# Kernel tuning notes

Hardware: AMD Instinct MI355X
Metric: run time of the kernel (lower is better)

## Reference

```python
import jax, jax.numpy as jnp
import numpy as np
from jax import lax

B, N, D, S, K = 8, 4096, 61, 1024, 32
MLP = (64, 64, 128)
WN = (3, 8, 8, 16)  # WeightNet: 3 -> 8 -> 8 -> 16
EPS = 1e-5


def _gather(p, idx):
    # p: [B, N, C], idx: [B, ...] -> [B, ..., C]
    return jax.vmap(lambda pb, ib: pb[ib])(p, idx)


def _fps(xyz, npoint, key):
    # farthest point sampling, xyz: [B, N, 3] -> idx [B, npoint]
    b, n, _ = xyz.shape
    start = jax.random.randint(key, (b,), 0, n)
    def step(carry, _):
        dmin, far = carry
        centroid = jnp.take_along_axis(xyz, far[:, None, None], axis=1)  # [B,1,3]
        d = jnp.sum((xyz - centroid) ** 2, -1)                            # [B,N]
        dmin = jnp.minimum(dmin, d)
        return (dmin, jnp.argmax(dmin, -1)), far
    _, idxs = lax.scan(step, (jnp.full((b, n), 1e10, xyz.dtype), start), None, length=npoint)
    return idxs.T  # [B, npoint]


def _sqdist(a, b):
    # a: [B,S,3], b: [B,N,3] -> [B,S,N]
    return (jnp.sum(a ** 2, -1)[:, :, None] + jnp.sum(b ** 2, -1)[:, None, :]
            - 2.0 * jnp.einsum('bsc,bnc->bsn', a, b))


def _bn_relu(x, g, be):
    # channels-last BN (training-mode batch stats, biased var) + ReLU
    axes = tuple(range(x.ndim - 1))
    m = x.mean(axes, keepdims=True)
    v = x.var(axes, keepdims=True)
    return jax.nn.relu(g * (x - m) * lax.rsqrt(v + EPS) + be)


def _forward(xyz, points, mlp_p, wn_p, lin_w, lin_b, bnl_g, bnl_b):
    xyz_t = xyz.transpose(0, 2, 1)    # [B,N,3]
    pts = points.transpose(0, 2, 1)   # [B,N,D]
    xyz_sg = lax.stop_gradient(xyz_t)  # index computations carry no grads (as in torch)
    fps_idx = _fps(xyz_sg, S, jax.random.key(42))  # [B,S]
    new_xyz = _gather(xyz_t, fps_idx)              # [B,S,3]
    idx = lax.top_k(-_sqdist(lax.stop_gradient(new_xyz), xyz_sg), K)[1]  # [B,S,K]
    g_norm = _gather(xyz_t, idx) - new_xyz[:, :, None, :]                # [B,S,K,3]
    feat = jnp.concatenate([g_norm, _gather(pts, idx)], -1)              # [B,S,K,3+D]
    for w, b, g, be in mlp_p:
        feat = _bn_relu(jnp.einsum('bskc,oc->bsko', feat, w) + b, g, be)
    wts = g_norm
    for w, b, g, be in wn_p:
        wts = _bn_relu(jnp.einsum('bskc,oc->bsko', wts, w) + b, g, be)   # [B,S,K,16]
    # [B,S,C,K] @ [B,S,K,16] -> [B,S,C,16] -> [B,S,C*16] (C-major flatten, as torch .view)
    agg = jnp.einsum('bskc,bskw->bscw', feat, wts).reshape(B, S, -1)
    out = agg @ lin_w.T + lin_b                                          # [B,S,128]
    m = out.mean((0, 1), keepdims=True)  # BatchNorm1d over batch and spatial
    v = out.var((0, 1), keepdims=True)
    out = jax.nn.relu(bnl_g * (out - m) * lax.rsqrt(v + EPS) + bnl_b)
    return new_xyz.transpose(0, 2, 1), out.transpose(0, 2, 1)  # [B,3,S], [B,128,S]


def setup_inputs() -> dict:
    key = jax.random.key(0)
    ks = iter(jax.random.split(key, 64))
    inp = {"xyz": jax.random.normal(next(ks), (B, 3, N), jnp.float32),
           "points": jax.random.normal(next(ks), (B, D, N), jnp.float32)}
    mlp_in = (3 + D,) + MLP[:-1]
    for i, (ci, co) in enumerate(zip(mlp_in, MLP)):
        inp[f"mlp_w{i}"] = jax.random.normal(next(ks), (co, ci), jnp.float32) / np.float32(np.sqrt(ci))
        inp[f"mlp_b{i}"] = jnp.zeros((co,), jnp.float32)
        inp[f"mlp_g{i}"] = jnp.ones((co,), jnp.float32)
        inp[f"mlp_be{i}"] = jnp.zeros((co,), jnp.float32)
    for i, (ci, co) in enumerate(zip(WN[:-1], WN[1:])):
        inp[f"wn_w{i}"] = jax.random.normal(next(ks), (co, ci), jnp.float32) / np.float32(np.sqrt(ci))
        inp[f"wn_b{i}"] = jnp.zeros((co,), jnp.float32)
        inp[f"wn_g{i}"] = jnp.ones((co,), jnp.float32)
        inp[f"wn_be{i}"] = jnp.zeros((co,), jnp.float32)
    fin = 16 * MLP[-1]
    inp["lin_w"] = jax.random.normal(next(ks), (MLP[-1], fin), jnp.float32) / np.float32(np.sqrt(fin))
    inp["lin_b"] = jnp.zeros((MLP[-1],), jnp.float32)
    inp["bnl_g"] = jnp.ones((MLP[-1],), jnp.float32)
    inp["bnl_b"] = jnp.zeros((MLP[-1],), jnp.float32)
    return inp


def reference(xyz, points, mlp_w0, mlp_b0, mlp_g0, mlp_be0, mlp_w1, mlp_b1, mlp_g1, mlp_be1, mlp_w2, mlp_b2, mlp_g2, mlp_be2, wn_w0, wn_b0, wn_g0, wn_be0, wn_w1, wn_b1, wn_g1, wn_be1, wn_w2, wn_b2, wn_g2, wn_be2, lin_w, lin_b, bnl_g, bnl_b):
    mlp_p = [(mlp_w0, mlp_b0, mlp_g0, mlp_be0),
             (mlp_w1, mlp_b1, mlp_g1, mlp_be1),
             (mlp_w2, mlp_b2, mlp_g2, mlp_be2)]
    wn_p = [(wn_w0, wn_b0, wn_g0, wn_be0),
            (wn_w1, wn_b1, wn_g1, wn_be1),
            (wn_w2, wn_b2, wn_g2, wn_be2)]
    return _forward(xyz, points, mlp_p, wn_p, lin_w, lin_b, bnl_g, bnl_b)
```

## Files before the change

kernel.cpp:

```cpp
#include <hip/hip_runtime.h>
#include <cstdint>
#include <cstddef>


constexpr int B_ = 8, N_ = 4096, D_ = 61, S_ = 1024, K_ = 32;
constexpr int P_ = B_ * S_ * K_;
constexpr int BS_ = B_ * S_;

constexpr size_t OFF_STATS  = 0;
constexpr size_t OFF_FPSIDX = 8192;
constexpr size_t OFF_NEWXYZ = 40960;
constexpr size_t OFF_KNN    = 139264;
constexpr size_t OFF_PT     = 1187840;
constexpr size_t OFF_Y01    = 9183232;
constexpr size_t OFF_Y2     = 76292096;
constexpr size_t OFF_W01    = 210509824;
constexpr size_t OFF_W2B    = 218898432;
constexpr size_t OFF_OUTPRE = 235675648;

static inline uint32_t rotl32(uint32_t x, int r){ return (x << r) | (x >> (32 - r)); }
static void tf2x32(uint32_t k0, uint32_t k1, uint32_t x0, uint32_t x1,
                   uint32_t* o0, uint32_t* o1){
  uint32_t ks[3] = {k0, k1, k0 ^ k1 ^ 0x1BD11BDAu};
  x0 += ks[0]; x1 += ks[1];
  const int RA[4] = {13,15,26,6}, RB[4] = {17,29,16,24};
  for (int i = 0; i < 5; ++i){
    const int* R = (i & 1) ? RB : RA;
    for (int j = 0; j < 4; ++j){ x0 += x1; x1 = rotl32(x1, R[j]); x1 ^= x0; }
    x0 += ks[(i+1)%3]; x1 += ks[(i+2)%3] + (uint32_t)(i+1);
  }
  *o0 = x0; *o1 = x1;
}
struct StartIdx { int v[8]; };
static StartIdx compute_starts(){
  uint32_t ka, kb;
  tf2x32(0u, 42u, 0u, 1u, &ka, &kb);
  StartIdx s;
  for (int i = 0; i < 8; ++i){
    uint32_t b1, b2;
    tf2x32(ka, kb, 0u, (uint32_t)i, &b1, &b2);
    s.v[i] = (int)((b1 ^ b2) & 4095u);
  }
  return s;
}

__global__ __launch_bounds__(64) void tr_kernel(const float* __restrict__ pts,
                                                float* __restrict__ pT){
  __shared__ float tile[61][65];
  const int b = blockIdx.x >> 6;
  const int n0 = (blockIdx.x & 63) * 64;
  const int t = threadIdx.x;
  for (int d = 0; d < 61; ++d)
    tile[d][t] = pts[((size_t)b*61 + d)*N_ + n0 + t];
  __syncthreads();
  float* dst = pT + ((size_t)b*N_ + n0 + t)*61;
  for (int d = 0; d < 61; ++d) dst[d] = tile[d][t];
}

#define REP8(M) M(0) M(1) M(2) M(3) M(4) M(5) M(6) M(7)

__global__ __launch_bounds__(512, 1) void fps_kernel(const float* __restrict__ xyz,
                                                     StartIdx st,
                                                     float* __restrict__ new_xyz,
                                                     float* __restrict__ out_xyz){
  const int b = blockIdx.x, tid = threadIdx.x;
  const int lane = tid & 63, wv = tid >> 6;
  const float* xb = xyz + (size_t)b*3*N_;
  __shared__ float4 pts4[N_];
  __shared__ unsigned long long slots[2][8];

#define LOADP(i) \
  float px##i = xb[tid + 512*(i)]; \
  float py##i = xb[N_ + tid + 512*(i)]; \
  float pz##i = xb[2*N_ + tid + 512*(i)]; \
  float dm##i = 1e10f; \
  pts4[tid + 512*(i)] = make_float4(px##i, py##i, pz##i, 0.f);
  REP8(LOADP)
#undef LOADP
  __syncthreads();

  const int start = st.v[b];
  float4 c4 = pts4[start];
  float cx = c4.x, cy = c4.y, cz = c4.z;

  int par = 0;
  for (int s = 0; s < S_; ++s){
    if (tid == 0){
      new_xyz[((size_t)b*S_ + s)*3 + 0] = cx;
      new_xyz[((size_t)b*S_ + s)*3 + 1] = cy;
      new_xyz[((size_t)b*S_ + s)*3 + 2] = cz;
      out_xyz[(size_t)b*3*S_ + s]        = cx;
      out_xyz[(size_t)b*3*S_ + S_ + s]   = cy;
      out_xyz[(size_t)b*3*S_ + 2*S_ + s] = cz;
    }
#define UPD(i) \
    unsigned long long key##i; { \
      float dx = __fsub_rn(px##i, cx), dy = __fsub_rn(py##i, cy), dz = __fsub_rn(pz##i, cz); \
      float d  = __fadd_rn(__fadd_rn(__fmul_rn(dx,dx), __fmul_rn(dy,dy)), __fmul_rn(dz,dz)); \
      dm##i = fminf(dm##i, d); \
      key##i = ((unsigned long long)__float_as_uint(dm##i) << 32) \
             | (unsigned int)(~(unsigned int)(tid + 512*(i))); }
    REP8(UPD)
#undef UPD
    unsigned long long t0 = key0 > key1 ? key0 : key1;
    unsigned long long t1 = key2 > key3 ? key2 : key3;
    unsigned long long t2 = key4 > key5 ? key4 : key5;
    unsigned long long t3 = key6 > key7 ? key6 : key7;
    unsigned long long u0 = t0 > t1 ? t0 : t1;
    unsigned long long u1 = t2 > t3 ? t2 : t3;
    unsigned long long k  = u0 > u1 ? u0 : u1;
#pragma unroll
    for (int off = 32; off >= 1; off >>= 1){
      unsigned long long o = __shfl_xor(k, off);
      if (o > k) k = o;
    }
    if (lane == 0) slots[par][wv] = k;
    __syncthreads();
    unsigned long long bk = slots[par][0];
    { unsigned long long v1 = slots[par][1]; if (v1 > bk) bk = v1;
      unsigned long long v2 = slots[par][2]; if (v2 > bk) bk = v2;
      unsigned long long v3 = slots[par][3]; if (v3 > bk) bk = v3;
      unsigned long long v4 = slots[par][4]; if (v4 > bk) bk = v4;
      unsigned long long v5 = slots[par][5]; if (v5 > bk) bk = v5;
      unsigned long long v6 = slots[par][6]; if (v6 > bk) bk = v6;
      unsigned long long v7 = slots[par][7]; if (v7 > bk) bk = v7; }
    const int winner = (int)(~(unsigned int)bk) & (N_ - 1);
    float4 w4 = pts4[winner];
    cx = w4.x; cy = w4.y; cz = w4.z;
    par ^= 1;
  }
}
#undef REP8

__global__ __launch_bounds__(256) void knn_kernel(const float* __restrict__ xyz,
                                                  const float* __restrict__ nxyz,
                                                  int* __restrict__ knn_idx){
  __shared__ float dist[4][4096];
  const int wv = threadIdx.x >> 6, lane = threadIdx.x & 63;
  const int q = blockIdx.x*4 + wv;
  const int b = q >> 10;
  const float* xb = xyz + (size_t)b*3*N_;
  const float ax = nxyz[(size_t)q*3], ay = nxyz[(size_t)q*3+1], az = nxyz[(size_t)q*3+2];
  const float sa = __fadd_rn(__fadd_rn(__fmul_rn(ax,ax), __fmul_rn(ay,ay)), __fmul_rn(az,az));
  float* dw = dist[wv];
  float lv = 3.4e38f; int ln = 0;
  for (int i = 0; i < 64; ++i){
    int n = i*64 + lane;
    float x = xb[n], y = xb[N_+n], z = xb[2*N_+n];
    float sb  = __fadd_rn(__fadd_rn(__fmul_rn(x,x), __fmul_rn(y,y)), __fmul_rn(z,z));
    float dot = __fadd_rn(__fadd_rn(__fmul_rn(ax,x), __fmul_rn(ay,y)), __fmul_rn(az,z));
    float d   = __fsub_rn(__fadd_rn(sa, sb), __fmul_rn(2.f, dot));
    dw[n] = d;
    if (d < lv){ lv = d; ln = n; }
  }
  __syncthreads();
  int myout = 0;
  for (int r = 0; r < 32; ++r){
    float gv = lv; int gn = ln;
#pragma unroll
    for (int off = 32; off >= 1; off >>= 1){
      float ov = __shfl_xor(gv, off); int on = __shfl_xor(gn, off);
      if (ov < gv || (ov == gv && on < gn)){ gv = ov; gn = on; }
    }
    if (lane == r) myout = gn;
    const int col = gn & 63, row = gn >> 6;
    float v = dw[lane*64 + col];
    if (lane == row){ v = 3.4e38f; dw[lane*64 + col] = 3.4e38f; }
    float nv = v; int nn = lane*64 + col;
#pragma unroll
    for (int off = 32; off >= 1; off >>= 1){
      float ov = __shfl_xor(nv, off); int on = __shfl_xor(nn, off);
      if (ov < nv || (ov == nv && on < nn)){ nv = ov; nn = on; }
    }
    if (lane == col){ lv = nv; ln = nn; }
  }
  if (lane < 32) knn_idx[(size_t)q*32 + lane] = myout;
}

__global__ __launch_bounds__(256, 2) void m0_kernel(const float* __restrict__ pT,
                                                    const float* __restrict__ xyz,
                                                    const float* __restrict__ nxyz,
                                                    const int* __restrict__ knn_idx,
                                                    const float* __restrict__ w,
                                                    const float* __restrict__ bias,
                                                    float* __restrict__ y){
  __shared__ float Wt[4096]; __shared__ float bb[64];
  for (int t = threadIdx.x; t < 4096; t += 256){ int o = t >> 6, c = t & 63; Wt[c*64+o] = w[o*64+c]; }
  if (threadIdx.x < 64) bb[threadIdx.x] = bias[threadIdx.x];
  __syncthreads();
  const int p = blockIdx.x*256 + threadIdx.x;
  const int b = p >> 15, s = (p & 32767) >> 5;
  const int n = knn_idx[p];
  float in[64];
  {
    const float* xb = xyz + (size_t)b*3*N_;
    const int q = (b << 10) + s;
    in[0] = xb[n]       - nxyz[(size_t)q*3];
    in[1] = xb[N_+n]    - nxyz[(size_t)q*3+1];
    in[2] = xb[2*N_+n]  - nxyz[(size_t)q*3+2];
    const float* pr = pT + ((size_t)b*N_ + n)*61;
#pragma unroll
    for (int d = 0; d < 61; ++d) in[3+d] = pr[d];
  }
  float acc[64];
#pragma unroll
  for (int o = 0; o < 64; ++o) acc[o] = bb[o];
#pragma unroll
  for (int c = 0; c < 64; ++c){
    float x = in[c];
#pragma unroll
    for (int o = 0; o < 64; o += 4){
      float4 w4 = *reinterpret_cast<const float4*>(&Wt[c*64+o]);
      acc[o]   += x*w4.x; acc[o+1] += x*w4.y; acc[o+2] += x*w4.z; acc[o+3] += x*w4.w;
    }
  }
#pragma unroll
  for (int o = 0; o < 64; ++o) y[(size_t)o*P_ + p] = acc[o];
}

__global__ __launch_bounds__(256) void stats_kernel(const float* __restrict__ y,
                                                    double* __restrict__ st, int C){
  const int c = blockIdx.x % C, chunk = blockIdx.x / C;
  const float* row = y + (size_t)c*P_ + (size_t)chunk*32768;
  double s = 0.0, q = 0.0;
  for (int i = threadIdx.x; i < 32768; i += 256){ double v = row[i]; s += v; q += v*v; }
  __shared__ double ss[256], qq[256];
  ss[threadIdx.x] = s; qq[threadIdx.x] = q; __syncthreads();
  for (int w = 128; w >= 1; w >>= 1){
    if (threadIdx.x < w){ ss[threadIdx.x] += ss[threadIdx.x+w]; qq[threadIdx.x] += qq[threadIdx.x+w]; }
    __syncthreads();
  }
  if (threadIdx.x == 0){ atomicAdd(&st[c*2], ss[0]); atomicAdd(&st[c*2+1], qq[0]); }
}

__device__ __forceinline__ void bn_coeff(const double* st, const float* g, const float* be,
                                         int c, double cnt, float* sc, float* sh){
  double mean = st[c*2] / cnt;
  double var  = st[c*2+1] / cnt - mean*mean;
  double scale = (double)g[c] / sqrt(var + 1e-5);
  *sc = (float)scale; *sh = (float)((double)be[c] - mean*scale);
}

__global__ __launch_bounds__(256, 2) void m1_kernel(float* __restrict__ y,
                                                    const float* __restrict__ w,
                                                    const float* __restrict__ bias,
                                                    const double* __restrict__ st,
                                                    const float* __restrict__ g,
                                                    const float* __restrict__ be){
  __shared__ float Wt[4096]; __shared__ float bb[64], sc[64], sh[64];
  for (int t = threadIdx.x; t < 4096; t += 256){ int o = t >> 6, c = t & 63; Wt[c*64+o] = w[o*64+c]; }
  if (threadIdx.x < 64){
    bn_coeff(st, g, be, threadIdx.x, (double)P_, &sc[threadIdx.x], &sh[threadIdx.x]);
    bb[threadIdx.x] = bias[threadIdx.x];
  }
  __syncthreads();
  const int p = blockIdx.x*256 + threadIdx.x;
  float in[64];
#pragma unroll
  for (int c = 0; c < 64; ++c){
    float x = y[(size_t)c*P_ + p];
    in[c] = fmaxf(0.f, fmaf(x, sc[c], sh[c]));
  }
  float acc[64];
#pragma unroll
  for (int o = 0; o < 64; ++o) acc[o] = bb[o];
#pragma unroll
  for (int c = 0; c < 64; ++c){
    float x = in[c];
#pragma unroll
    for (int o = 0; o < 64; o += 4){
      float4 w4 = *reinterpret_cast<const float4*>(&Wt[c*64+o]);
      acc[o]   += x*w4.x; acc[o+1] += x*w4.y; acc[o+2] += x*w4.z; acc[o+3] += x*w4.w;
    }
  }
#pragma unroll
  for (int o = 0; o < 64; ++o) y[(size_t)o*P_ + p] = acc[o];
}

__global__ __launch_bounds__(256, 2) void m2_kernel(const float* __restrict__ y1,
                                                    float* __restrict__ y2,
                                                    const float* __restrict__ w,
                                                    const float* __restrict__ bias,
                                                    const double* __restrict__ st,
                                                    const float* __restrict__ g,
                                                    const float* __restrict__ be){
  __shared__ float Wt[4096]; __shared__ float bb[64], sc[64], sh[64];
  const int half = blockIdx.y;
  for (int t = threadIdx.x; t < 4096; t += 256){
    int o = t >> 6, c = t & 63;
    Wt[c*64+o] = w[(size_t)(half*64+o)*64 + c];
  }
  if (threadIdx.x < 64){
    bn_coeff(st, g, be, threadIdx.x, (double)P_, &sc[threadIdx.x], &sh[threadIdx.x]);
    bb[threadIdx.x] = bias[half*64 + threadIdx.x];
  }
  __syncthreads();
  const int p = blockIdx.x*256 + threadIdx.x;
  float in[64];
#pragma unroll
  for (int c = 0; c < 64; ++c){
    float x = y1[(size_t)c*P_ + p];
    in[c] = fmaxf(0.f, fmaf(x, sc[c], sh[c]));
  }
  float acc[64];
#pragma unroll
  for (int o = 0; o < 64; ++o) acc[o] = bb[o];
#pragma unroll
  for (int c = 0; c < 64; ++c){
    float x = in[c];
#pragma unroll
    for (int o = 0; o < 64; o += 4){
      float4 w4 = *reinterpret_cast<const float4*>(&Wt[c*64+o]);
      acc[o]   += x*w4.x; acc[o+1] += x*w4.y; acc[o+2] += x*w4.z; acc[o+3] += x*w4.w;
    }
  }
#pragma unroll
  for (int o = 0; o < 64; ++o) y2[(size_t)(half*64+o)*P_ + p] = acc[o];
}

__global__ __launch_bounds__(256) void w0_kernel(const float* __restrict__ xyz,
                                                 const float* __restrict__ nxyz,
                                                 const int* __restrict__ knn_idx,
                                                 const float* __restrict__ w,
                                                 const float* __restrict__ bias,
                                                 float* __restrict__ wb){
  __shared__ float Wl[24], bb[8];
  if (threadIdx.x < 24) Wl[threadIdx.x] = w[threadIdx.x];
  if (threadIdx.x < 8)  bb[threadIdx.x] = bias[threadIdx.x];
  __syncthreads();
  const int p = blockIdx.x*256 + threadIdx.x;
  const int b = p >> 15, s = (p & 32767) >> 5;
  const int n = knn_idx[p];
  const float* xb = xyz + (size_t)b*3*N_;
  const int q = (b << 10) + s;
  float gx = xb[n]      - nxyz[(size_t)q*3];
  float gy = xb[N_+n]   - nxyz[(size_t)q*3+1];
  float gz = xb[2*N_+n] - nxyz[(size_t)q*3+2];
#pragma unroll
  for (int o = 0; o < 8; ++o){
    float a = bb[o] + gx*Wl[o*3] + gy*Wl[o*3+1] + gz*Wl[o*3+2];
    wb[(size_t)o*P_ + p] = a;
  }
}

__global__ __launch_bounds__(256) void w1_kernel(float* __restrict__ wb,
                                                 const float* __restrict__ w,
                                                 const float* __restrict__ bias,
                                                 const double* __restrict__ st,
                                                 const float* __restrict__ g,
                                                 const float* __restrict__ be){
  __shared__ float Wl[64], bb[8], sc[8], sh[8];
  if (threadIdx.x < 64) Wl[threadIdx.x] = w[threadIdx.x];
  if (threadIdx.x < 8){
    bn_coeff(st, g, be, threadIdx.x, (double)P_, &sc[threadIdx.x], &sh[threadIdx.x]);
    bb[threadIdx.x] = bias[threadIdx.x];
  }
  __syncthreads();
  const int p = blockIdx.x*256 + threadIdx.x;
  float in[8];
#pragma unroll
  for (int c = 0; c < 8; ++c){
    float x = wb[(size_t)c*P_ + p];
    in[c] = fmaxf(0.f, fmaf(x, sc[c], sh[c]));
  }
  float acc[8];
#pragma unroll
  for (int o = 0; o < 8; ++o){
    float a = bb[o];
#pragma unroll
    for (int c = 0; c < 8; ++c) a += in[c]*Wl[o*8+c];
    acc[o] = a;
  }
#pragma unroll
  for (int o = 0; o < 8; ++o) wb[(size_t)o*P_ + p] = acc[o];
}

__global__ __launch_bounds__(256) void w2_kernel(const float* __restrict__ wb,
                                                 float* __restrict__ wb2,
                                                 const float* __restrict__ w,
                                                 const float* __restrict__ bias,
                                                 const double* __restrict__ st,
                                                 const float* __restrict__ g,
                                                 const float* __restrict__ be){
  __shared__ float Wl[128], bb[16], sc[8], sh[8];
  if (threadIdx.x < 128) Wl[threadIdx.x] = w[threadIdx.x];
  if (threadIdx.x < 8)
    bn_coeff(st, g, be, threadIdx.x, (double)P_, &sc[threadIdx.x], &sh[threadIdx.x]);
  if (threadIdx.x < 16) bb[threadIdx.x] = bias[threadIdx.x];
  __syncthreads();
  const int p = blockIdx.x*256 + threadIdx.x;
  float in[8];
#pragma unroll
  for (int c = 0; c < 8; ++c){
    float x = wb[(size_t)c*P_ + p];
    in[c] = fmaxf(0.f, fmaf(x, sc[c], sh[c]));
  }
#pragma unroll
  for (int o = 0; o < 16; ++o){
    float a = bb[o];
#pragma unroll
    for (int c = 0; c < 8; ++c) a += in[c]*Wl[o*8+c];
    wb2[(size_t)o*P_ + p] = a;
  }
}

__global__ __launch_bounds__(256) void agg_kernel(const float* __restrict__ y2,
                                                  const float* __restrict__ wb2,
                                                  const double* __restrict__ st2,
                                                  const float* __restrict__ g2,
                                                  const float* __restrict__ be2,
                                                  const double* __restrict__ stw,
                                                  const float* __restrict__ gw,
                                                  const float* __restrict__ bew,
                                                  float* __restrict__ agg){
  __shared__ float f[32*132];
  __shared__ float wt[32*16];
  __shared__ float sc2[128], sh2[128], scw[16], shw[16];
  const int t = threadIdx.x;
  if (t < 128) bn_coeff(st2, g2, be2, t, (double)P_, &sc2[t], &sh2[t]);
  if (t < 16)  bn_coeff(stw, gw, bew, t, (double)P_, &scw[t], &shw[t]);
  __syncthreads();
  const int bs = blockIdx.x;
  const size_t p0 = (size_t)bs * 32;
  for (int e = t; e < 4096; e += 256){
    int c = e >> 5, k = e & 31;
    float x = y2[(size_t)c*P_ + p0 + k];
    f[k*132 + c] = fmaxf(0.f, fmaf(x, sc2[c], sh2[c]));
  }
  for (int e = t; e < 512; e += 256){
    int w = e >> 5, k = e & 31;
    float x = wb2[(size_t)w*P_ + p0 + k];
    wt[k*16 + w] = fmaxf(0.f, fmaf(x, scw[w], shw[w]));
  }
  __syncthreads();
  const int c = t >> 1, wp = (t & 1) * 8;
  float a0=0,a1=0,a2=0,a3=0,a4=0,a5=0,a6=0,a7=0;
#pragma unroll
  for (int k = 0; k < 32; ++k){
    float fv = f[k*132 + c];
    float4 u = *reinterpret_cast<const float4*>(&wt[k*16 + wp]);
    float4 v = *reinterpret_cast<const float4*>(&wt[k*16 + wp + 4]);
    a0 += fv*u.x; a1 += fv*u.y; a2 += fv*u.z; a3 += fv*u.w;
    a4 += fv*v.x; a5 += fv*v.y; a6 += fv*v.z; a7 += fv*v.w;
  }
  float* dst = agg + (size_t)bs*2048 + c*16 + wp;
  *reinterpret_cast<float4*>(dst)     = make_float4(a0,a1,a2,a3);
  *reinterpret_cast<float4*>(dst + 4) = make_float4(a4,a5,a6,a7);
}

__global__ __launch_bounds__(256) void lin_kernel(const float* __restrict__ agg,
                                                  const float* __restrict__ lw,
                                                  const float* __restrict__ lb,
                                                  float* __restrict__ outp){
  __shared__ float A[32*33];
  __shared__ float Wl[32*128];
  __shared__ float lbs[128];
  const int t = threadIdx.x;
  const int r0 = blockIdx.x * 32;
  if (t < 128) lbs[t] = lb[t];
  const int c_lane = t & 31, rg = t >> 5;
  float acc[4][4];
#pragma unroll
  for (int i = 0; i < 4; ++i)
#pragma unroll
    for (int j = 0; j < 4; ++j) acc[i][j] = 0.f;

  for (int kk0 = 0; kk0 < 2048; kk0 += 32){
    __syncthreads();
    {
      int r = t >> 3, kq = (t & 7) * 4;
      float4 v = *reinterpret_cast<const float4*>(&agg[(size_t)(r0 + r)*2048 + kk0 + kq]);
      A[r*33 + kq]   = v.x; A[r*33 + kq+1] = v.y; A[r*33 + kq+2] = v.z; A[r*33 + kq+3] = v.w;
    }
    {
#pragma unroll
      for (int u = 0; u < 4; ++u){
        int fid = t + 256*u;
        int o = fid >> 3, kq = (fid & 7) * 4;
        float4 v = *reinterpret_cast<const float4*>(&lw[(size_t)o*2048 + kk0 + kq]);
        Wl[(kq  )*128 + o] = v.x; Wl[(kq+1)*128 + o] = v.y;
        Wl[(kq+2)*128 + o] = v.z; Wl[(kq+3)*128 + o] = v.w;
      }
    }
    __syncthreads();
#pragma unroll 8
    for (int kk = 0; kk < 32; ++kk){
      float a0 = A[(rg*4+0)*33 + kk], a1 = A[(rg*4+1)*33 + kk],
            a2 = A[(rg*4+2)*33 + kk], a3 = A[(rg*4+3)*33 + kk];
#pragma unroll
      for (int j = 0; j < 4; ++j){
        float wv = Wl[kk*128 + c_lane + 32*j];
        acc[0][j] += a0*wv; acc[1][j] += a1*wv; acc[2][j] += a2*wv; acc[3][j] += a3*wv;
      }
    }
  }
  __syncthreads();
#pragma unroll
  for (int i = 0; i < 4; ++i)
#pragma unroll
    for (int j = 0; j < 4; ++j){
      int o = c_lane + 32*j;
      outp[(size_t)(r0 + rg*4 + i)*128 + o] = acc[i][j] + lbs[o];
    }
}

__global__ __launch_bounds__(128) void statsF_kernel(const float* __restrict__ outp,
                                                     double* __restrict__ st){
  const int c = threadIdx.x;
  const int r0 = blockIdx.x * 128;
  double s = 0.0, q = 0.0;
  for (int r = 0; r < 128; ++r){
    double v = outp[(size_t)(r0 + r)*128 + c];
    s += v; q += v*v;
  }
  atomicAdd(&st[c*2], s); atomicAdd(&st[c*2+1], q);
}

__global__ __launch_bounds__(256) void final_kernel(const float* __restrict__ outp,
                                                    const double* __restrict__ st,
                                                    const float* __restrict__ g,
                                                    const float* __restrict__ be,
                                                    float* __restrict__ out){
  const int gid = blockIdx.x*256 + threadIdx.x;
  const int s = gid & 1023, o = (gid >> 10) & 127, b = gid >> 17;
  float sc, sh;
  bn_coeff(st, g, be, o, (double)BS_, &sc, &sh);
  float x = outp[((size_t)(b << 10) + s)*128 + o];
  out[gid] = fmaxf(0.f, fmaf(x, sc, sh));
}

extern "C" void kernel_launch(void* const* d_in, const int* in_sizes, int n_in,
                              void* d_out, int out_size, void* d_ws, size_t ws_size,
                              hipStream_t stream){
  (void)in_sizes; (void)n_in; (void)out_size; (void)ws_size;
  const float* xyz    = (const float*)d_in[0];
  const float* points = (const float*)d_in[1];
  const float* mw0 = (const float*)d_in[2],  *mb0 = (const float*)d_in[3],
             * mg0 = (const float*)d_in[4],  *me0 = (const float*)d_in[5];
  const float* mw1 = (const float*)d_in[6],  *mb1 = (const float*)d_in[7],
             * mg1 = (const float*)d_in[8],  *me1 = (const float*)d_in[9];
  const float* mw2 = (const float*)d_in[10], *mb2 = (const float*)d_in[11],
             * mg2 = (const float*)d_in[12], *me2 = (const float*)d_in[13];
  const float* ww0 = (const float*)d_in[14], *wb0 = (const float*)d_in[15],
             * wg0 = (const float*)d_in[16], *we0 = (const float*)d_in[17];
  const float* ww1 = (const float*)d_in[18], *wb1 = (const float*)d_in[19],
             * wg1 = (const float*)d_in[20], *we1 = (const float*)d_in[21];
  const float* ww2 = (const float*)d_in[22], *wb2_ = (const float*)d_in[23],
             * wg2 = (const float*)d_in[24], *we2 = (const float*)d_in[25];
  const float* lw  = (const float*)d_in[26], *lb  = (const float*)d_in[27];
  const float* fg  = (const float*)d_in[28], *fb  = (const float*)d_in[29];

  char* ws = (char*)d_ws;
  double* ST0 = (double*)(ws + OFF_STATS);
  double* ST1 = (double*)(ws + OFF_STATS + 1024);
  double* ST2 = (double*)(ws + OFF_STATS + 2048);
  double* SW0 = (double*)(ws + OFF_STATS + 4096);
  double* SW1 = (double*)(ws + OFF_STATS + 4224);
  double* SW2 = (double*)(ws + OFF_STATS + 4352);
  double* STF = (double*)(ws + OFF_STATS + 4608);
  float* nxyz   = (float*)(ws + OFF_NEWXYZ);
  int*   knnidx = (int*)(ws + OFF_KNN);
  float* pT     = (float*)(ws + OFF_PT);
  float* y01    = (float*)(ws + OFF_Y01);
  float* y2     = (float*)(ws + OFF_Y2);
  float* w01    = (float*)(ws + OFF_W01);
  float* w2b    = (float*)(ws + OFF_W2B);
  float* aggbuf = (float*)(ws + OFF_Y01);
  float* outpre = (float*)(ws + OFF_OUTPRE);

  float* out_xyz  = (float*)d_out;
  float* out_feat = (float*)d_out + (size_t)B_*3*S_;

  hipMemsetAsync(ws + OFF_STATS, 0, 8192, stream);

  tr_kernel<<<dim3(B_*64), dim3(64), 0, stream>>>(points, pT);

  StartIdx st = compute_starts();
  fps_kernel<<<dim3(B_), dim3(512), 0, stream>>>(xyz, st, nxyz, out_xyz);

  knn_kernel<<<dim3(BS_/4), dim3(256), 0, stream>>>(xyz, nxyz, knnidx);

  m0_kernel<<<dim3(P_/256), dim3(256), 0, stream>>>(pT, xyz, nxyz, knnidx, mw0, mb0, y01);
  stats_kernel<<<dim3(64*8), dim3(256), 0, stream>>>(y01, ST0, 64);
  m1_kernel<<<dim3(P_/256), dim3(256), 0, stream>>>(y01, mw1, mb1, ST0, mg0, me0);
  stats_kernel<<<dim3(64*8), dim3(256), 0, stream>>>(y01, ST1, 64);
  m2_kernel<<<dim3(P_/256, 2), dim3(256), 0, stream>>>(y01, y2, mw2, mb2, ST1, mg1, me1);
  stats_kernel<<<dim3(128*8), dim3(256), 0, stream>>>(y2, ST2, 128);

  w0_kernel<<<dim3(P_/256), dim3(256), 0, stream>>>(xyz, nxyz, knnidx, ww0, wb0, w01);
  stats_kernel<<<dim3(8*8), dim3(256), 0, stream>>>(w01, SW0, 8);
  w1_kernel<<<dim3(P_/256), dim3(256), 0, stream>>>(w01, ww1, wb1, SW0, wg0, we0);
  stats_kernel<<<dim3(8*8), dim3(256), 0, stream>>>(w01, SW1, 8);
  w2_kernel<<<dim3(P_/256), dim3(256), 0, stream>>>(w01, w2b, ww2, wb2_, SW1, wg1, we1);
  stats_kernel<<<dim3(16*8), dim3(256), 0, stream>>>(w2b, SW2, 16);

  agg_kernel<<<dim3(BS_), dim3(256), 0, stream>>>(y2, w2b, ST2, mg2, me2, SW2, wg2, we2, aggbuf);
  lin_kernel<<<dim3(BS_/32), dim3(256), 0, stream>>>(aggbuf, lw, lb, outpre);
  statsF_kernel<<<dim3(BS_/128), dim3(128), 0, stream>>>(outpre, STF);
  final_kernel<<<dim3((B_*128*S_)/256), dim3(256), 0, stream>>>(outpre, STF, fg, fb, out_feat);
}
```

Measured before the change: 1.689 ms.

## Use DPP wave reductions in FPS and kNN, pad point features, vectorize loads

FPS replaces the 64-bit shuffle argmax with a float DPP max followed by a DPP min over candidate indices. kNN packs distance and index into order-preserving 64-bit keys, reduces them with DPP, and skews its shared-memory distance layout to avoid bank conflicts. Point features are padded to a 64-float stride so the first MLP can use float4 loads, and the stats kernel reads float4. The workspace offsets are rearranged and the output buffer is aliased onto the W01 region, which could conflict if both are live at the same time.

```diff
diff --git a/kernel.cpp b/kernel.cpp
--- a/kernel.cpp
+++ b/kernel.cpp
@@ -8,15 +8,14 @@
 constexpr int BS_ = B_ * S_;
 
 constexpr size_t OFF_STATS  = 0;
-constexpr size_t OFF_FPSIDX = 8192;
-constexpr size_t OFF_NEWXYZ = 40960;
-constexpr size_t OFF_KNN    = 139264;
-constexpr size_t OFF_PT     = 1187840;
-constexpr size_t OFF_Y01    = 9183232;
-constexpr size_t OFF_Y2     = 76292096;
-constexpr size_t OFF_W01    = 210509824;
-constexpr size_t OFF_W2B    = 218898432;
-constexpr size_t OFF_OUTPRE = 235675648;
+constexpr size_t OFF_NEWXYZ = 8192;
+constexpr size_t OFF_KNN    = 106496;
+constexpr size_t OFF_PT     = 1155072;
+constexpr size_t OFF_Y01    = 9543680;
+constexpr size_t OFF_Y2     = 76652544;
+constexpr size_t OFF_W01    = 210870272;
+constexpr size_t OFF_W2B    = 219258880;
+constexpr size_t OFF_OUTPRE = OFF_W01;
 
 static inline uint32_t rotl32(uint32_t x, int r){ return (x << r) | (x >> (32 - r)); }
 static void tf2x32(uint32_t k0, uint32_t k1, uint32_t x0, uint32_t x1,
@@ -44,6 +43,59 @@
   return s;
 }
 
+template<int C>
+__device__ __forceinline__ float dpp_max_f32_step(float x){
+  int t = __builtin_amdgcn_update_dpp(0, (int)__float_as_uint(x), C, 0xf, 0xf, true);
+  return fmaxf(x, __uint_as_float((unsigned)t));
+}
+__device__ __forceinline__ float dpp_wave_max_f32(float x){
+  x = dpp_max_f32_step<0x111>(x);
+  x = dpp_max_f32_step<0x112>(x);
+  x = dpp_max_f32_step<0x114>(x);
+  x = dpp_max_f32_step<0x118>(x);
+  x = dpp_max_f32_step<0x142>(x);
+  x = dpp_max_f32_step<0x143>(x);
+  return __uint_as_float((unsigned)__builtin_amdgcn_readlane((int)__float_as_uint(x), 63));
+}
+template<int C>
+__device__ __forceinline__ unsigned dpp_min_u32_step(unsigned x){
+  int t = __builtin_amdgcn_update_dpp(-1, (int)x, C, 0xf, 0xf, false);
+  unsigned u = (unsigned)t;
+  return u < x ? u : x;
+}
+__device__ __forceinline__ unsigned dpp_wave_min_u32(unsigned x){
+  x = dpp_min_u32_step<0x111>(x);
+  x = dpp_min_u32_step<0x112>(x);
+  x = dpp_min_u32_step<0x114>(x);
+  x = dpp_min_u32_step<0x118>(x);
+  x = dpp_min_u32_step<0x142>(x);
+  x = dpp_min_u32_step<0x143>(x);
+  return (unsigned)__builtin_amdgcn_readlane((int)x, 63);
+}
+template<int C>
+__device__ __forceinline__ unsigned long long dpp_min_u64_step(unsigned long long k){
+  unsigned lo = (unsigned)k, hi = (unsigned)(k >> 32);
+  unsigned olo = (unsigned)__builtin_amdgcn_update_dpp(-1, (int)lo, C, 0xf, 0xf, false);
+  unsigned ohi = (unsigned)__builtin_amdgcn_update_dpp(-1, (int)hi, C, 0xf, 0xf, false);
+  unsigned long long o = ((unsigned long long)ohi << 32) | olo;
+  return o < k ? o : k;
+}
+__device__ __forceinline__ unsigned long long dpp_wave_min_u64(unsigned long long k){
+  k = dpp_min_u64_step<0x111>(k);
+  k = dpp_min_u64_step<0x112>(k);
+  k = dpp_min_u64_step<0x114>(k);
+  k = dpp_min_u64_step<0x118>(k);
+  k = dpp_min_u64_step<0x142>(k);
+  k = dpp_min_u64_step<0x143>(k);
+  unsigned lo = (unsigned)__builtin_amdgcn_readlane((int)(unsigned)k, 63);
+  unsigned hi = (unsigned)__builtin_amdgcn_readlane((int)(unsigned)(k >> 32), 63);
+  return ((unsigned long long)hi << 32) | lo;
+}
+__device__ __forceinline__ unsigned ordf(float f){
+  unsigned u = __float_as_uint(f);
+  return u ^ (unsigned)(((int)u >> 31) | 0x80000000);
+}
+
 __global__ __launch_bounds__(64) void tr_kernel(const float* __restrict__ pts,
                                                 float* __restrict__ pT){
   __shared__ float tile[61][65];
@@ -53,8 +105,8 @@
   for (int d = 0; d < 61; ++d)
     tile[d][t] = pts[((size_t)b*61 + d)*N_ + n0 + t];
   __syncthreads();
-  float* dst = pT + ((size_t)b*N_ + n0 + t)*61;
-  for (int d = 0; d < 61; ++d) dst[d] = tile[d][t];
+  for (int r = 0; r < 64; ++r)
+    pT[((size_t)b*N_ + n0 + r)*64 + t] = (t < 61) ? tile[t][r] : 0.f;
 }
 
 #define REP8(M) M(0) M(1) M(2) M(3) M(4) M(5) M(6) M(7)
@@ -93,28 +145,24 @@
       out_xyz[(size_t)b*3*S_ + S_ + s]   = cy;
       out_xyz[(size_t)b*3*S_ + 2*S_ + s] = cz;
     }
-#define UPD(i) \
-    unsigned long long key##i; { \
+#define UPD(i) { \
       float dx = __fsub_rn(px##i, cx), dy = __fsub_rn(py##i, cy), dz = __fsub_rn(pz##i, cz); \
       float d  = __fadd_rn(__fadd_rn(__fmul_rn(dx,dx), __fmul_rn(dy,dy)), __fmul_rn(dz,dz)); \
-      dm##i = fminf(dm##i, d); \
-      key##i = ((unsigned long long)__float_as_uint(dm##i) << 32) \
-             | (unsigned int)(~(unsigned int)(tid + 512*(i))); }
+      dm##i = fminf(dm##i, d); }
     REP8(UPD)
 #undef UPD
-    unsigned long long t0 = key0 > key1 ? key0 : key1;
-    unsigned long long t1 = key2 > key3 ? key2 : key3;
-    unsigned long long t2 = key4 > key5 ? key4 : key5;
-    unsigned long long t3 = key6 > key7 ? key6 : key7;
-    unsigned long long u0 = t0 > t1 ? t0 : t1;
-    unsigned long long u1 = t2 > t3 ? t2 : t3;
-    unsigned long long k  = u0 > u1 ? u0 : u1;
-#pragma unroll
-    for (int off = 32; off >= 1; off >>= 1){
-      unsigned long long o = __shfl_xor(k, off);
-      if (o > k) k = o;
-    }
-    if (lane == 0) slots[par][wv] = k;
+    float m01 = fmaxf(dm0, dm1), m23 = fmaxf(dm2, dm3);
+    float m45 = fmaxf(dm4, dm5), m67 = fmaxf(dm6, dm7);
+    float lmax = fmaxf(fmaxf(m01, m23), fmaxf(m45, m67));
+    float wmax = dpp_wave_max_f32(lmax);
+    unsigned cand = 0xFFFFFFFFu;
+#define CAND(i) cand = (dm##i == wmax) ? (unsigned)(tid + 512*(i)) : cand;
+    CAND(7) CAND(6) CAND(5) CAND(4) CAND(3) CAND(2) CAND(1) CAND(0)
+#undef CAND
+    unsigned widx = dpp_wave_min_u32(cand);
+    if (lane == 63)
+      slots[par][wv] = ((unsigned long long)__float_as_uint(wmax) << 32)
+                     | (unsigned long long)(unsigned)(~widx);
     __syncthreads();
     unsigned long long bk = slots[par][0];
     { unsigned long long v1 = slots[par][1]; if (v1 > bk) bk = v1;
@@ -124,7 +172,7 @@
       unsigned long long v5 = slots[par][5]; if (v5 > bk) bk = v5;
       unsigned long long v6 = slots[par][6]; if (v6 > bk) bk = v6;
       unsigned long long v7 = slots[par][7]; if (v7 > bk) bk = v7; }
-    const int winner = (int)(~(unsigned int)bk) & (N_ - 1);
+    const int winner = (int)(~(unsigned)bk) & (N_ - 1);
     float4 w4 = pts4[winner];
     cx = w4.x; cy = w4.y; cz = w4.z;
     par ^= 1;
@@ -143,36 +191,31 @@
   const float ax = nxyz[(size_t)q*3], ay = nxyz[(size_t)q*3+1], az = nxyz[(size_t)q*3+2];
   const float sa = __fadd_rn(__fadd_rn(__fmul_rn(ax,ax), __fmul_rn(ay,ay)), __fmul_rn(az,az));
   float* dw = dist[wv];
-  float lv = 3.4e38f; int ln = 0;
+  unsigned long long kk = ~0ull;
   for (int i = 0; i < 64; ++i){
     int n = i*64 + lane;
     float x = xb[n], y = xb[N_+n], z = xb[2*N_+n];
     float sb  = __fadd_rn(__fadd_rn(__fmul_rn(x,x), __fmul_rn(y,y)), __fmul_rn(z,z));
     float dot = __fadd_rn(__fadd_rn(__fmul_rn(ax,x), __fmul_rn(ay,y)), __fmul_rn(az,z));
     float d   = __fsub_rn(__fadd_rn(sa, sb), __fmul_rn(2.f, dot));
-    dw[n] = d;
-    if (d < lv){ lv = d; ln = n; }
+    dw[i*64 + ((lane + i) & 63)] = d;
+    unsigned long long key = ((unsigned long long)ordf(d) << 32) | (unsigned)n;
+    if (key < kk) kk = key;
   }
   __syncthreads();
   int myout = 0;
   for (int r = 0; r < 32; ++r){
-    float gv = lv; int gn = ln;
-#pragma unroll
-    for (int off = 32; off >= 1; off >>= 1){
-      float ov = __shfl_xor(gv, off); int on = __shfl_xor(gn, off);
-      if (ov < gv || (ov == gv && on < gn)){ gv = ov; gn = on; }
-    }
+    unsigned long long g = dpp_wave_min_u64(kk);
+    const int gn = (int)(g & 0xFFFFFFFFull);
     if (lane == r) myout = gn;
     const int col = gn & 63, row = gn >> 6;
-    float v = dw[lane*64 + col];
-    if (lane == row){ v = 3.4e38f; dw[lane*64 + col] = 3.4e38f; }
-    float nv = v; int nn = lane*64 + col;
-#pragma unroll
-    for (int off = 32; off >= 1; off >>= 1){
-      float ov = __shfl_xor(nv, off); int on = __shfl_xor(nn, off);
-      if (ov < nv || (ov == nv && on < nn)){ nv = ov; nn = on; }
-    }
-    if (lane == col){ lv = nv; ln = nn; }
+    const int a = lane*64 + ((col + lane) & 63);
+    float v = dw[a];
+    if (lane == row){ v = 3.4e38f; dw[a] = 3.4e38f; }
+    unsigned long long nk = ((unsigned long long)ordf(v) << 32)
+                          | (unsigned)(lane*64 + col);
+    nk = dpp_wave_min_u64(nk);
+    if (lane == col) kk = nk;
   }
   if (lane < 32) knn_idx[(size_t)q*32 + lane] = myout;
 }
@@ -198,9 +241,13 @@
     in[0] = xb[n]       - nxyz[(size_t)q*3];
     in[1] = xb[N_+n]    - nxyz[(size_t)q*3+1];
     in[2] = xb[2*N_+n]  - nxyz[(size_t)q*3+2];
-    const float* pr = pT + ((size_t)b*N_ + n)*61;
-#pragma unroll
-    for (int d = 0; d < 61; ++d) in[3+d] = pr[d];
+    const float* pr = pT + ((size_t)b*N_ + n)*64;
+#pragma unroll
+    for (int d = 0; d < 60; d += 4){
+      float4 v = *reinterpret_cast<const float4*>(&pr[d]);
+      in[3+d] = v.x; in[4+d] = v.y; in[5+d] = v.z; in[6+d] = v.w;
+    }
+    in[63] = pr[60];
   }
   float acc[64];
 #pragma unroll
@@ -221,9 +268,13 @@
 __global__ __launch_bounds__(256) void stats_kernel(const float* __restrict__ y,
                                                     double* __restrict__ st, int C){
   const int c = blockIdx.x % C, chunk = blockIdx.x / C;
-  const float* row = y + (size_t)c*P_ + (size_t)chunk*32768;
+  const float4* row4 = reinterpret_cast<const float4*>(y + (size_t)c*P_ + (size_t)chunk*32768);
   double s = 0.0, q = 0.0;
-  for (int i = threadIdx.x; i < 32768; i += 256){ double v = row[i]; s += v; q += v*v; }
+  for (int i = threadIdx.x; i < 8192; i += 256){
+    float4 v = row4[i];
+    s += (double)v.x + (double)v.y + (double)v.z + (double)v.w;
+    q += (double)v.x*v.x + (double)v.y*v.y + (double)v.z*v.z + (double)v.w*v.w;
+  }
   __shared__ double ss[256], qq[256];
   ss[threadIdx.x] = s; qq[threadIdx.x] = q; __syncthreads();
   for (int w = 128; w >= 1; w >>= 1){
```

After: 1.558 ms. -7.7%, faster.
